# Performance work log

Measured on AMD Instinct MI355X. Metric: run time of the kernel, lower is better.

## Reference

```python
import jax, jax.numpy as jnp
from jax import lax
import numpy as np

B, N, XS, LAT = 16, 400000, 256, 10


def setup_inputs() -> dict:
    key = jax.random.key(0)
    ks = jax.random.split(key, 9)
    flow = 2.0 * jax.random.normal(ks[0], (B, N, 3), jnp.float32)
    x = jax.random.normal(ks[1], (B, XS, XS), jnp.float32)
    values = jax.random.normal(ks[2], (N,), jnp.float32)
    # near-identity rotation matrices so most splatted points stay in-grid
    rotations = jnp.eye(3, dtype=jnp.float32)[None] + 0.05 * jax.random.normal(ks[3], (B, 3, 3), jnp.float32)
    shifts = 2.0 * jax.random.normal(ks[4], (B, 2), jnp.float32)
    w1 = 0.001 * jax.random.normal(ks[5], (XS * XS, LAT), jnp.float32)
    b1 = jnp.zeros((LAT,), jnp.float32)
    w2 = 0.1 * jax.random.normal(ks[6], (LAT, 2), jnp.float32)
    b2 = jnp.zeros((2,), jnp.float32)
    inds = jax.random.randint(ks[7], (N, 3), 0, XS, dtype=jnp.int32)
    return dict(flow=flow, x=x, values=values, rotations=rotations, shifts=shifts,
                w1=w1, b1=b1, w2=w2, b2=b2, inds=inds, xsize=XS)


def _gaussian_blur3(imgs):
    # dm_pix.gaussian_blur(sigma=1.0, kernel_size=3): separable, SAME (zero) padding
    g = jnp.exp(jnp.asarray(-0.5, imgs.dtype))
    k = jnp.stack([g, jnp.asarray(1.0, imgs.dtype), g])
    k = k / k.sum()
    xi = imgs[:, None]  # (B,1,H,W)
    kh = k.reshape(1, 1, 3, 1)
    kw = k.reshape(1, 1, 1, 3)
    xi = lax.conv_general_dilated(xi, kh, (1, 1), 'SAME')
    xi = lax.conv_general_dilated(xi, kw, (1, 1), 'SAME')
    return xi[:, 0]


def reference(flow, x, values, rotations, shifts, w1, b1, w2, b2, inds, xsize):
    factor = 0.5 * xsize
    # (1,N,3) coords in (z->x order as in source), center, deform
    coords = jnp.stack([inds[:, 2], inds[:, 1], inds[:, 0]], axis=1)[None].astype(flow.dtype)
    coords = coords - factor + flow                       # (B,N,3)
    coords = jnp.einsum('bnc,brc->bnr', coords, rotations)  # coords @ R^T
    coords = coords[..., :2] - shifts[:, None, :] + factor  # (B,N,2)
    c_sampling = jnp.stack([coords[..., 1], coords[..., 0]], axis=2)  # swap -> (row, col)

    bamp = values[None, :]                                # (1,N) broadcast over B
    bposf = jnp.floor(c_sampling)
    bposi = bposf.astype(jnp.int32)                       # (B,N,2)
    frac = c_sampling - bposf                             # fractional parts
    f0, f1 = frac[:, :, 0], frac[:, :, 1]
    a0 = bamp * (1.0 - f0) * (1.0 - f1)
    a1 = bamp * f0 * (1.0 - f1)
    a2 = bamp * f0 * f1
    a3 = bamp * (1.0 - f0) * f1
    bamp_all = jnp.concatenate([a0, a1, a2, a3], axis=1)  # (B,4N)
    bposi_all = jnp.concatenate([bposi,
                                 bposi + jnp.array((1, 0), jnp.int32),
                                 bposi + jnp.array((1, 1), jnp.int32),
                                 bposi + jnp.array((0, 1), jnp.int32)], axis=1)  # (B,4N,2)

    images = jnp.zeros((flow.shape[0], xsize, xsize), flow.dtype)

    def scatter_img(image, pos_i, amp_i):
        return image.at[pos_i[:, 0], pos_i[:, 1]].add(amp_i)

    images = jax.vmap(scatter_img)(images, bposi_all, bamp_all)
    images = _gaussian_blur3(images)

    # ImageAdjustment: per-image scalar gain/offset from conditioning image x
    h = jax.nn.relu(x.reshape(x.shape[0], -1) @ w1 + b1)
    ab = h @ w2 + b2                                      # (B,2)
    a, b = ab[:, 0], ab[:, 1]
    images = a[:, None, None] * images + b[:, None, None]
    # ctf_type == 'none' -> ctfFilter skipped
    return images
```

## Files before the change

kernel.cpp:

```cpp
#include <hip/hip_runtime.h>

#define XS     256
#define XS2    65536
#define LAT    10
#define BR     8
#define NG     (XS / BR)
#define NBINS  512
#define P1     4096
#define K_MAX  7
#define BINCAP 15360
#define SPLIT  2
#define CELLW  128
#define QS     256.0f
#define INVQS  (1.0f / 256.0f)

__device__ __forceinline__ void lds_add_u64(unsigned long long* p,
                                            unsigned long long v) {
    __hip_atomic_fetch_add(p, v, __ATOMIC_RELAXED, __HIP_MEMORY_SCOPE_WORKGROUP);
}

__device__ __forceinline__ unsigned long long pack4(int q0, int q1, int q2, int q3) {
    return (unsigned long long)((long long)q0 + ((long long)q1 << 16) +
                                ((long long)q2 << 32) + ((long long)q3 << 48));
}

__device__ __forceinline__ void compute_rc(const float* __restrict__ flow,
                                           const int* __restrict__ inds,
                                           const float* __restrict__ rot,
                                           const float* __restrict__ shifts,
                                           int b, int n, int N,
                                           int& r, int& c, float& f0, float& f1) {
    const float* R = rot + b * 9;
    float r00 = R[0], r01 = R[1], r02 = R[2];
    float r10 = R[3], r11 = R[4], r12 = R[5];
    float s0 = shifts[b * 2 + 0], s1 = shifts[b * 2 + 1];
    size_t fo = ((size_t)b * N + n) * 3;
    float fw0 = flow[fo + 0], fw1 = flow[fo + 1], fw2 = flow[fo + 2];
    float v0 = (float)inds[n * 3 + 2] - 128.0f + fw0;
    float v1 = (float)inds[n * 3 + 1] - 128.0f + fw1;
    float v2 = (float)inds[n * 3 + 0] - 128.0f + fw2;
    float p0 = fmaf(v0, r00, fmaf(v1, r01, fmaf(v2, r02, 128.0f - s0)));
    float p1 = fmaf(v0, r10, fmaf(v1, r11, fmaf(v2, r12, 128.0f - s1)));
    float cs0 = p1, cs1 = p0;
    float ff0 = floorf(cs0), ff1 = floorf(cs1);
    r = (int)ff0; c = (int)ff1;
    f0 = cs0 - ff0; f1 = cs1 - ff1;
}

__device__ __forceinline__ void corner_q(int* __restrict__ Q, int rr, int cc, float a) {
    if (rr >= -XS && rr < XS && cc >= -XS && cc < XS) {
        int q = __float2int_rn(a * QS);
        if (q) atomicAdd(&Q[((rr + XS) & (XS - 1)) * XS + ((cc + XS) & (XS - 1))], q);
    }
}

__device__ __forceinline__ bool is_fast(int r) {
    return (r >= -XS) && (r <= XS - 2) && (r != -1);
}

__device__ __forceinline__ void rec_fallback_q(unsigned long long rec, int bin,
                                               int* __restrict__ qimg) {
    unsigned w = (unsigned)rec;
    float amp = __uint_as_float((unsigned)(rec >> 32));
    int b = bin >> 5, g = bin & 31;
    int rig = w & 7, wc = (w >> 3) & 255;
    int wr = g * BR + rig;
    float f0 = (float)((w >> 13) & 511) * (1.0f / 512.0f);
    float f1 = (float)((w >> 22) & 511) * (1.0f / 512.0f);
    float g0 = 1.0f - f0, g1 = 1.0f - f1;
    int* Q = qimg + (size_t)b * XS2;
    if (w & (1u << 11)) {
        int q00 = __float2int_rn(amp * g0 * g1 * QS);
        int q10 = __float2int_rn(amp * f0 * g1 * QS);
        if (q00) atomicAdd(&Q[wr * XS + wc], q00);
        if (q10) atomicAdd(&Q[(wr + 1) * XS + wc], q10);
    }
    if (w & (1u << 12)) {
        int wc1 = (wc + 1) & 255;
        int q01 = __float2int_rn(amp * g0 * f1 * QS);
        int q11 = __float2int_rn(amp * f0 * f1 * QS);
        if (q01) atomicAdd(&Q[wr * XS + wc1], q01);
        if (q11) atomicAdd(&Q[(wr + 1) * XS + wc1], q11);
    }
}

__global__ void init_kernel(uint4* __restrict__ p, int n4) {
    int i = blockIdx.x * blockDim.x + threadIdx.x;
    int stride = gridDim.x * blockDim.x;
    uint4 z; z.x = 0u; z.y = 0u; z.z = 0u; z.w = 0u;
    for (; i < n4; i += stride) p[i] = z;
}

__device__ __forceinline__ void mlp_block(const float* __restrict__ x,
                                          const float* __restrict__ w1,
                                          float* __restrict__ hraw, int id) {
    int t = threadIdx.x;
    int b = id / LAT, l = id - b * LAT;
    const float* xb = x + (size_t)b * XS2;
    float acc = 0.0f;
#pragma unroll 8
    for (int j = 0; j < 256; j++) {
        int e = j * 256 + t;
        acc += xb[e] * w1[(size_t)e * LAT + l];
    }
#pragma unroll
    for (int off = 32; off > 0; off >>= 1) acc += __shfl_down(acc, off);
    __shared__ float red[4];
    if ((t & 63) == 0) red[t >> 6] = acc;
    __syncthreads();
    if (t == 0) hraw[b * LAT + l] = (red[0] + red[1]) + (red[2] + red[3]);
}

__global__ void __launch_bounds__(256, 6)
place_kernel(const float* __restrict__ flow,
             const float* __restrict__ values,
             const int* __restrict__ inds,
             const float* __restrict__ rot,
             const float* __restrict__ shifts,
             const float* __restrict__ x,
             const float* __restrict__ w1,
             float* __restrict__ hraw,
             unsigned* __restrict__ gcursor,
             unsigned long long* __restrict__ recs,
             int* __restrict__ qimg,
             int N, int TI, int IPB, int B) {
    int t = threadIdx.x;

    if (blockIdx.x >= P1) {
        mlp_block(x, w1, hraw, blockIdx.x - P1);
        return;
    }

    __shared__ unsigned lcnt[NBINS];
    __shared__ unsigned lbase[NBINS];
    lcnt[t] = 0; lcnt[t + 256] = 0;
    __syncthreads();

    unsigned long long rec[K_MAX];
    unsigned meta[K_MAX];
    int s = blockIdx.x * IPB;
    int e = min(s + IPB, TI);
    int b0 = s / N;
    int bBound = (b0 + 1) * N;

#pragma unroll
    for (int k = 0; k < K_MAX; k++) {
        meta[k] = 0xFFFFFFFFu;
        int i = s + t + k * 256;
        if (i < e) {
            int b = (i < bBound) ? b0 : b0 + 1;
            int n = i - b * N;
            int r, c; float f0, f1;
            compute_rc(flow, inds, rot, shifts, b, n, N, r, c, f0, f1);
            float amp = values[n];
            if (is_fast(r)) {
                int wr = (r + XS) & (XS - 1);
                int wc = c & (XS - 1);
                unsigned cv0 = (c >= -XS && c < XS) ? 1u : 0u;
                unsigned cv1 = (c + 1 >= -XS && c + 1 < XS) ? 1u : 0u;
                unsigned q0 = min(511u, (unsigned)(f0 * 512.0f + 0.5f));
                unsigned q1 = min(511u, (unsigned)(f1 * 512.0f + 0.5f));
                unsigned word = (unsigned)(wr & 7) | ((unsigned)wc << 3) |
                                (cv0 << 11) | (cv1 << 12) | (q0 << 13) | (q1 << 22);
                int bin = b * NG + (wr >> 3);
                unsigned rank = atomicAdd(&lcnt[bin], 1u);
                meta[k] = (unsigned)bin | (rank << 9);
                rec[k] = ((unsigned long long)__float_as_uint(amp) << 32) | word;
            } else {
                float g0 = 1.0f - f0, g1 = 1.0f - f1;
                int* Q = qimg + (size_t)b * XS2;
                corner_q(Q, r,     c,     amp * g0 * g1);
                corner_q(Q, r + 1, c,     amp * f0 * g1);
                corner_q(Q, r + 1, c + 1, amp * f0 * f1);
                corner_q(Q, r,     c + 1, amp * g0 * f1);
            }
        }
    }
    __syncthreads();

    for (int bin = t; bin < NBINS; bin += 256) {
        unsigned cn = lcnt[bin];
        lbase[bin] = cn ? atomicAdd(&gcursor[bin], cn) : 0u;
    }
    __syncthreads();

#pragma unroll
    for (int k = 0; k < K_MAX; k++) {
        unsigned m = meta[k];
        if (m != 0xFFFFFFFFu) {
            unsigned bin = m & (NBINS - 1);
            unsigned idx = lbase[bin] + (m >> 9);
            if (idx < BINCAP) recs[(size_t)bin * BINCAP + idx] = rec[k];
            else rec_fallback_q(rec[k], (int)bin, qimg);
        }
    }
}

__global__ void __launch_bounds__(256)
accum_kernel(const unsigned long long* __restrict__ recs,
             const unsigned* __restrict__ gcursor,
             float* __restrict__ reps,
             float* __restrict__ aprons, int B) {
    int bin = blockIdx.x >> 1, sp = blockIdx.x & 1;
    int b = bin >> 5, g = bin & 31;
    __shared__ unsigned long long teven[BR * CELLW];
    __shared__ unsigned long long todd[BR * CELLW];
    int t = threadIdx.x;
    for (int k = t; k < BR * CELLW; k += 256) { teven[k] = 0ull; todd[k] = 0ull; }
    __syncthreads();

    unsigned cnt = min(gcursor[bin], (unsigned)BINCAP);
    unsigned lo = (unsigned)(((unsigned long long)cnt * sp) / SPLIT);
    unsigned hi = (unsigned)(((unsigned long long)cnt * (sp + 1)) / SPLIT);
    const unsigned long long* rb = recs + (size_t)bin * BINCAP;

    for (unsigned i = lo + t; i < hi; i += 256) {
        unsigned long long rc = rb[i];
        unsigned w = (unsigned)rc;
        float amp = __uint_as_float((unsigned)(rc >> 32));
        int rig = w & 7, wc = (w >> 3) & 255;
        float f0 = (float)((w >> 13) & 511) * (1.0f / 512.0f);
        float f1 = (float)((w >> 22) & 511) * (1.0f / 512.0f);
        float g0 = 1.0f - f0, g1 = 1.0f - f1;
        bool cv0 = (w >> 11) & 1, cv1 = (w >> 12) & 1;
        int q00 = cv0 ? __float2int_rn(amp * g0 * g1 * QS) : 0;
        int q10 = cv0 ? __float2int_rn(amp * f0 * g1 * QS) : 0;
        int q01 = cv1 ? __float2int_rn(amp * g0 * f1 * QS) : 0;
        int q11 = cv1 ? __float2int_rn(amp * f0 * f1 * QS) : 0;
        unsigned long long inc = pack4(q00, q10, q01, q11);
        unsigned long long* tile = (wc & 1) ? todd : teven;
        lds_add_u64(&tile[rig * CELLW + (wc >> 1)], inc);
    }
    __syncthreads();

    int c = t;
    int je = c >> 1;
    int jo = (c & 1) ? (c >> 1) : (((c + 254) & 255) >> 1);
    bool e_lo = (c & 1) == 0;
    bool o_lo = (c & 1) == 1;
    float* rep = reps + ((size_t)sp * B + b) * XS2;
    float carry = 0.0f;
#pragma unroll
    for (int rig = 0; rig < BR; rig++) {
        long long se = (long long)teven[rig * CELLW + je];
        int e0 = (int)(short)(se & 0xffff); se = (se - e0) >> 16;
        int e1 = (int)(short)(se & 0xffff); se = (se - e1) >> 16;
        int e2 = (int)(short)(se & 0xffff); se = (se - e2) >> 16;
        int e3 = (int)se;
        long long so = (long long)todd[rig * CELLW + jo];
        int o0 = (int)(short)(so & 0xffff); so = (so - o0) >> 16;
        int o1 = (int)(short)(so & 0xffff); so = (so - o1) >> 16;
        int o2 = (int)(short)(so & 0xffff); so = (so - o2) >> 16;
        int o3 = (int)so;
        float r0 = (e_lo ? (float)e0 : (float)e2) + (o_lo ? (float)o0 : (float)o2);
        float r1 = (e_lo ? (float)e1 : (float)e3) + (o_lo ? (float)o1 : (float)o3);
        rep[(g * BR + rig) * XS + c] = (carry + r0) * INVQS;
        carry = r1;
    }
    aprons[((size_t)bin * 2 + sp) * XS + c] = carry * INVQS;
}

__global__ void scatter_kernel(const float* __restrict__ flow,
                               const float* __restrict__ values,
                               const int* __restrict__ inds,
                               const float* __restrict__ rot,
                               const float* __restrict__ shifts,
                               int* __restrict__ qimg, int N) {
    int b = blockIdx.y;
    int n = blockIdx.x * blockDim.x + threadIdx.x;
    if (n >= N) return;
    int r, c; float f0, f1;
    compute_rc(flow, inds, rot, shifts, b, n, N, r, c, f0, f1);
    float amp = values[n];
    float g0 = 1.0f - f0, g1 = 1.0f - f1;
    int* Q = qimg + (size_t)b * XS2;
    corner_q(Q, r,     c,     amp * g0 * g1);
    corner_q(Q, r + 1, c,     amp * f0 * g1);
    corner_q(Q, r + 1, c + 1, amp * f0 * f1);
    corner_q(Q, r,     c + 1, amp * g0 * f1);
}

__global__ void mlp_kernel(const float* __restrict__ x,
                           const float* __restrict__ w1,
                           float* __restrict__ hraw) {
    mlp_block(x, w1, hraw, blockIdx.x);
}

__device__ __forceinline__ float S_load(const int* __restrict__ qimg,
                                        const float* __restrict__ reps,
                                        const float* __restrict__ aprons,
                                        int B, int b, int row, int c, int fast) {
    size_t o = (size_t)b * XS2 + row * XS + c;
    float v = (float)qimg[o] * INVQS;
    if (fast) {
        v += reps[o] + reps[(size_t)B * XS2 + o];
        if (row > 0 && (row & 7) == 0) {
            size_t bin = (size_t)b * NG + ((row >> 3) - 1);
            v += aprons[bin * 2 * XS + c] + aprons[(bin * 2 + 1) * XS + c];
        }
    }
    return v;
}

__global__ void blur_kernel(const int* __restrict__ qimg,
                            const float* __restrict__ reps,
                            const float* __restrict__ aprons,
                            const float* __restrict__ hraw,
                            const float* __restrict__ b1,
                            const float* __restrict__ w2,
                            const float* __restrict__ b2,
                            float* __restrict__ out, int B, int fast) {
    int b = blockIdx.y, r = blockIdx.x, c = threadIdx.x;
    float av = b2[0], bv = b2[1];
#pragma unroll
    for (int l = 0; l < LAT; l++) {
        float h = hraw[b * LAT + l] + b1[l];
        h = h > 0.0f ? h : 0.0f;
        av += h * w2[l * 2 + 0];
        bv += h * w2[l * 2 + 1];
    }
    const float g   = 0.6065306597126334f;
    const float inv = 1.0f / (1.0f + 2.0f * g);
    float up  = (r > 0)      ? S_load(qimg, reps, aprons, B, b, r - 1, c, fast) : 0.0f;
    float mid =                S_load(qimg, reps, aprons, B, b, r,     c, fast);
    float dn  = (r < XS - 1) ? S_load(qimg, reps, aprons, B, b, r + 1, c, fast) : 0.0f;
    float v = (g * (up + dn) + mid) * inv;
    __shared__ float row[XS + 2];
    row[c + 1] = v;
    if (c == 0) { row[0] = 0.0f; row[XS + 1] = 0.0f; }
    __syncthreads();
    float hh = (g * (row[c] + row[c + 2]) + v) * inv;
    out[(size_t)b * XS2 + (size_t)r * XS + c] = av * hh + bv;
}

extern "C" void kernel_launch(void* const* d_in, const int* in_sizes, int n_in,
                              void* d_out, int out_size, void* d_ws, size_t ws_size,
                              hipStream_t stream) {
    const float* flow   = (const float*)d_in[0];
    const float* x      = (const float*)d_in[1];
    const float* values = (const float*)d_in[2];
    const float* rot    = (const float*)d_in[3];
    const float* shifts = (const float*)d_in[4];
    const float* w1     = (const float*)d_in[5];
    const float* b1     = (const float*)d_in[6];
    const float* w2     = (const float*)d_in[7];
    const float* b2     = (const float*)d_in[8];
    const int*   inds   = (const int*)d_in[9];

    int N = in_sizes[2];
    int B = in_sizes[4] / 2;
    int TI  = B * N;
    int IPB = (TI + P1 - 1) / P1;

    size_t imgElems = (size_t)B * XS2;
    int*      qimg    = (int*)d_ws;
    float*    hraw    = (float*)(qimg + imgElems);
    unsigned* gcursor = (unsigned*)(hraw + 256);
    unsigned long long* recs = (unsigned long long*)(gcursor + NBINS);
    float*    reps    = (float*)(recs + (size_t)NBINS * BINCAP);
    float*    aprons  = reps + 2 * imgElems;
    size_t needed = (size_t)((char*)(aprons + (size_t)NBINS * 2 * XS) - (char*)d_ws);

    bool fast = (B * NG == NBINS) && (ws_size >= needed) && (IPB <= K_MAX * 256);

    int n4 = (int)((imgElems * sizeof(int) + 1024 + NBINS * 4) / 16);
    init_kernel<<<512, 256, 0, stream>>>((uint4*)d_ws, n4);

    if (fast) {
        place_kernel<<<P1 + B * LAT, 256, 0, stream>>>(flow, values, inds, rot, shifts,
                                                       x, w1, hraw, gcursor, recs, qimg,
                                                       N, TI, IPB, B);
        accum_kernel<<<NBINS * SPLIT, 256, 0, stream>>>(recs, gcursor, reps, aprons, B);
    } else {
        dim3 g1((N + 255) / 256, B);
        scatter_kernel<<<g1, 256, 0, stream>>>(flow, values, inds, rot, shifts, qimg, N);
        mlp_kernel<<<B * LAT, 256, 0, stream>>>(x, w1, hraw);
    }

    dim3 g3(XS, B);
    blur_kernel<<<g3, XS, 0, stream>>>(qimg, reps, aprons, hraw, b1, w2, b2,
                                       (float*)d_out, B, fast ? 1 : 0);
}
```

Baseline: 246.1 us.

## Stage binned records in LDS and write them contiguously per bin

The place kernel now keeps its records in LDS and uses a 64-bin local counter covering only the two batch images a block can touch. After a wave-level prefix scan it rebuilds the records grouped by bin, so the global stores become contiguous runs per bin instead of scattered 8-byte writes. The MLP blocks now launch first, and the occupancy hint in launch_bounds is removed. The change costs about 30 KB of LDS per block, which may lower occupancy, and adds an extra LDS pass and barrier. It also assumes IPB stays within RECSL.

```diff
diff --git a/kernel.cpp b/kernel.cpp
--- a/kernel.cpp
+++ b/kernel.cpp
@@ -8,6 +8,8 @@
 #define NBINS  512
 #define P1     4096
 #define K_MAX  7
+#define SLOTS  1792
+#define RECSL  1568
 #define BINCAP 15360
 #define SPLIT  2
 #define CELLW  128
@@ -111,7 +113,7 @@
     if (t == 0) hraw[b * LAT + l] = (red[0] + red[1]) + (red[2] + red[3]);
 }
 
-__global__ void __launch_bounds__(256, 6)
+__global__ void __launch_bounds__(256)
 place_kernel(const float* __restrict__ flow,
              const float* __restrict__ values,
              const int* __restrict__ inds,
@@ -126,27 +128,32 @@
              int N, int TI, int IPB, int B) {
     int t = threadIdx.x;
 
-    if (blockIdx.x >= P1) {
-        mlp_block(x, w1, hraw, blockIdx.x - P1);
+    if (blockIdx.x < (unsigned)(B * LAT)) {
+        mlp_block(x, w1, hraw, blockIdx.x);
         return;
     }
-
-    __shared__ unsigned lcnt[NBINS];
-    __shared__ unsigned lbase[NBINS];
-    lcnt[t] = 0; lcnt[t + 256] = 0;
-    __syncthreads();
-
-    unsigned long long rec[K_MAX];
-    unsigned meta[K_MAX];
-    int s = blockIdx.x * IPB;
+    int bid = blockIdx.x - B * LAT;
+
+    __shared__ unsigned long long recL[SLOTS];
+    __shared__ unsigned long long recS[RECSL];
+    __shared__ unsigned char bins8[SLOTS];
+    __shared__ unsigned char binR8[RECSL];
+    __shared__ unsigned lcnt[64];
+    __shared__ unsigned sbase[64];
+    __shared__ unsigned lbase[64];
+
+    if (t < 64) lcnt[t] = 0;
+    __syncthreads();
+
+    int s = bid * IPB;
     int e = min(s + IPB, TI);
     int b0 = s / N;
     int bBound = (b0 + 1) * N;
 
-#pragma unroll
     for (int k = 0; k < K_MAX; k++) {
-        meta[k] = 0xFFFFFFFFu;
-        int i = s + t + k * 256;
+        int slot = k * 256 + t;
+        int i = s + slot;
+        unsigned char bl = 0xFF;
         if (i < e) {
             int b = (i < bBound) ? b0 : b0 + 1;
             int n = i - b * N;
@@ -162,10 +169,10 @@
                 unsigned q1 = min(511u, (unsigned)(f1 * 512.0f + 0.5f));
                 unsigned word = (unsigned)(wr & 7) | ((unsigned)wc << 3) |
                                 (cv0 << 11) | (cv1 << 12) | (q0 << 13) | (q1 << 22);
-                int bin = b * NG + (wr >> 3);
-                unsigned rank = atomicAdd(&lcnt[bin], 1u);
-                meta[k] = (unsigned)bin | (rank << 9);
-                rec[k] = ((unsigned long long)__float_as_uint(amp) << 32) | word;
+                int local = (b - b0) * NG + (wr >> 3);
+                atomicAdd(&lcnt[local], 1u);
+                recL[slot] = ((unsigned long long)__float_as_uint(amp) << 32) | word;
+                bl = (unsigned char)local;
             } else {
                 float g0 = 1.0f - f0, g1 = 1.0f - f1;
                 int* Q = qimg + (size_t)b * XS2;
@@ -175,24 +182,46 @@
                 corner_q(Q, r,     c + 1, amp * g0 * f1);
             }
         }
-    }
-    __syncthreads();
-
-    for (int bin = t; bin < NBINS; bin += 256) {
-        unsigned cn = lcnt[bin];
-        lbase[bin] = cn ? atomicAdd(&gcursor[bin], cn) : 0u;
-    }
-    __syncthreads();
-
+        bins8[slot] = bl;
+    }
+    __syncthreads();
+
+    if (t < 64) {
+        unsigned cn = lcnt[t];
+        unsigned gb = 0;
+        if (cn) gb = atomicAdd(&gcursor[b0 * NG + t], cn);
+        lbase[t] = gb;
+        unsigned sc = cn;
 #pragma unroll
+        for (int off = 1; off < 64; off <<= 1) {
+            unsigned nv = __shfl_up(sc, off, 64);
+            if (t >= off) sc += nv;
+        }
+        sbase[t] = sc - cn;
+        lcnt[t] = 0;
+    }
+    __syncthreads();
+
     for (int k = 0; k < K_MAX; k++) {
-        unsigned m = meta[k];
-        if (m != 0xFFFFFFFFu) {
-            unsigned bin = m & (NBINS - 1);
-            unsigned idx = lbase[bin] + (m >> 9);
-            if (idx < BINCAP) recs[(size_t)bin * BINCAP + idx] = rec[k];
-            else rec_fallback_q(rec[k], (int)bin, qimg);
+        int slot = k * 256 + t;
+        unsigned bl = bins8[slot];
+        if (bl != 0xFFu) {
+            unsigned r2 = atomicAdd(&lcnt[bl], 1u);
+            unsigned q = sbase[bl] + r2;
+            recS[q] = recL[slot];
+            binR8[q] = (unsigned char)bl;
         }
+    }
+    __syncthreads();
+
+    unsigned total = sbase[63] + lcnt[63];
+    for (unsigned p = t; p < total; p += 256) {
+        unsigned long long rc = recS[p];
+        unsigned bl = binR8[p];
+        unsigned idx = lbase[bl] + (p - sbase[bl]);
+        int bing = b0 * NG + (int)bl;
+        if (idx < BINCAP) recs[(size_t)bing * BINCAP + idx] = rc;
+        else rec_fallback_q(rc, bing, qimg);
     }
 }
 
@@ -361,7 +390,7 @@
     float*    aprons  = reps + 2 * imgElems;
     size_t needed = (size_t)((char*)(aprons + (size_t)NBINS * 2 * XS) - (char*)d_ws);
 
-    bool fast = (B * NG == NBINS) && (ws_size >= needed) && (IPB <= K_MAX * 256);
+    bool fast = (B * NG == NBINS) && (ws_size >= needed) && (IPB <= RECSL);
 
     int n4 = (int)((imgElems * sizeof(int) + 1024 + NBINS * 4) / 16);
     init_kernel<<<512, 256, 0, stream>>>((uint4*)d_ws, n4);
```

Measured after the change: 216.7 us. 1.14x faster.

## Stage per-batch records in LDS and write bins out contiguously

Applied to the files above, without the earlier changes.

Place blocks now each cover one batch image (512 blocks per image) and keep records in shared-memory slots per row-bin instead of registers. After a per-bin global cursor reservation and a shuffle prefix scan, threads copy records out in a compacted order, so consecutive threads write consecutive addresses within a bin. This is meant to turn scattered 8-byte global stores into coalesced ones and drop the K_MAX register arrays so occupancy can rise to 8 waves per SIMD. The cost is extra LDS use, a binary search per output record, and more overflow traffic through the fallback path if a bin exceeds 64 records per block.

```diff
diff --git a/kernel.cpp b/kernel.cpp
--- a/kernel.cpp
+++ b/kernel.cpp
@@ -6,8 +6,8 @@
 #define BR     8
 #define NG     (XS / BR)
 #define NBINS  512
-#define P1     4096
-#define K_MAX  7
+#define SBB    512
+#define CAPB   64
 #define BINCAP 15360
 #define SPLIT  2
 #define CELLW  128
@@ -111,7 +111,7 @@
     if (t == 0) hraw[b * LAT + l] = (red[0] + red[1]) + (red[2] + red[3]);
 }
 
-__global__ void __launch_bounds__(256, 6)
+__global__ void __launch_bounds__(256, 8)
 place_kernel(const float* __restrict__ flow,
              const float* __restrict__ values,
              const int* __restrict__ inds,
@@ -123,76 +123,99 @@
              unsigned* __restrict__ gcursor,
              unsigned long long* __restrict__ recs,
              int* __restrict__ qimg,
-             int N, int TI, int IPB, int B) {
+             int N, int IPB, int B) {
     int t = threadIdx.x;
 
-    if (blockIdx.x >= P1) {
-        mlp_block(x, w1, hraw, blockIdx.x - P1);
+    if (blockIdx.x < (unsigned)(B * LAT)) {
+        mlp_block(x, w1, hraw, blockIdx.x);
         return;
     }
-
-    __shared__ unsigned lcnt[NBINS];
-    __shared__ unsigned lbase[NBINS];
-    lcnt[t] = 0; lcnt[t + 256] = 0;
-    __syncthreads();
-
-    unsigned long long rec[K_MAX];
-    unsigned meta[K_MAX];
-    int s = blockIdx.x * IPB;
-    int e = min(s + IPB, TI);
-    int b0 = s / N;
-    int bBound = (b0 + 1) * N;
-
+    int bid = blockIdx.x - B * LAT;
+    int b = bid >> 9;
+    int j = bid & (SBB - 1);
+
+    __shared__ unsigned long long slots[NG * CAPB];
+    __shared__ unsigned lcnt[NG];
+    __shared__ unsigned sbase[NG];
+    __shared__ unsigned lbase[NG];
+    if (t < NG) lcnt[t] = 0;
+    __syncthreads();
+
+    int s = b * N + j * IPB;
+    int e = min(s + IPB, (b + 1) * N);
+
+    const float* R = rot + b * 9;
+    float r00 = R[0], r01 = R[1], r02 = R[2];
+    float r10 = R[3], r11 = R[4], r12 = R[5];
+    float s0 = shifts[b * 2 + 0], s1 = shifts[b * 2 + 1];
+    int* Q = qimg + (size_t)b * XS2;
+
+    for (int i = s + t; i < e; i += 256) {
+        int n = i - b * N;
+        size_t fo = (size_t)i * 3;
+        float fw0 = flow[fo + 0], fw1 = flow[fo + 1], fw2 = flow[fo + 2];
+        float v0 = (float)inds[n * 3 + 2] - 128.0f + fw0;
+        float v1 = (float)inds[n * 3 + 1] - 128.0f + fw1;
+        float v2 = (float)inds[n * 3 + 0] - 128.0f + fw2;
+        float p0 = fmaf(v0, r00, fmaf(v1, r01, fmaf(v2, r02, 128.0f - s0)));
+        float p1 = fmaf(v0, r10, fmaf(v1, r11, fmaf(v2, r12, 128.0f - s1)));
+        float ff0 = floorf(p1), ff1 = floorf(p0);
+        int r = (int)ff0, c = (int)ff1;
+        float f0 = p1 - ff0, f1 = p0 - ff1;
+        float amp = values[n];
+        if (is_fast(r)) {
+            int wr = (r + XS) & (XS - 1);
+            int wc = c & (XS - 1);
+            unsigned cv0 = (c >= -XS && c < XS) ? 1u : 0u;
+            unsigned cv1 = (c + 1 >= -XS && c + 1 < XS) ? 1u : 0u;
+            unsigned q0 = min(511u, (unsigned)(f0 * 512.0f + 0.5f));
+            unsigned q1 = min(511u, (unsigned)(f1 * 512.0f + 0.5f));
+            unsigned word = (unsigned)(wr & 7) | ((unsigned)wc << 3) |
+                            (cv0 << 11) | (cv1 << 12) | (q0 << 13) | (q1 << 22);
+            unsigned long long rec =
+                ((unsigned long long)__float_as_uint(amp) << 32) | word;
+            int local = wr >> 3;
+            unsigned r2 = atomicAdd(&lcnt[local], 1u);
+            if (r2 < CAPB) slots[local * CAPB + r2] = rec;
+            else rec_fallback_q(rec, b * NG + local, qimg);
+        } else {
+            float g0 = 1.0f - f0, g1 = 1.0f - f1;
+            corner_q(Q, r,     c,     amp * g0 * g1);
+            corner_q(Q, r + 1, c,     amp * f0 * g1);
+            corner_q(Q, r + 1, c + 1, amp * f0 * f1);
+            corner_q(Q, r,     c + 1, amp * g0 * f1);
+        }
+    }
+    __syncthreads();
+
+    if (t < NG) {
+        unsigned cn = min(lcnt[t], (unsigned)CAPB);
+        unsigned gb = cn ? atomicAdd(&gcursor[b * NG + t], cn) : 0u;
+        lbase[t] = gb;
+        lcnt[t] = cn;
+        unsigned sc = cn;
 #pragma unroll
-    for (int k = 0; k < K_MAX; k++) {
-        meta[k] = 0xFFFFFFFFu;
-        int i = s + t + k * 256;
-        if (i < e) {
-            int b = (i < bBound) ? b0 : b0 + 1;
-            int n = i - b * N;
-            int r, c; float f0, f1;
-            compute_rc(flow, inds, rot, shifts, b, n, N, r, c, f0, f1);
-            float amp = values[n];
-            if (is_fast(r)) {
-                int wr = (r + XS) & (XS - 1);
-                int wc = c & (XS - 1);
-                unsigned cv0 = (c >= -XS && c < XS) ? 1u : 0u;
-                unsigned cv1 = (c + 1 >= -XS && c + 1 < XS) ? 1u : 0u;
-                unsigned q0 = min(511u, (unsigned)(f0 * 512.0f + 0.5f));
-                unsigned q1 = min(511u, (unsigned)(f1 * 512.0f + 0.5f));
-                unsigned word = (unsigned)(wr & 7) | ((unsigned)wc << 3) |
-                                (cv0 << 11) | (cv1 << 12) | (q0 << 13) | (q1 << 22);
-                int bin = b * NG + (wr >> 3);
-                unsigned rank = atomicAdd(&lcnt[bin], 1u);
-                meta[k] = (unsigned)bin | (rank << 9);
-                rec[k] = ((unsigned long long)__float_as_uint(amp) << 32) | word;
-            } else {
-                float g0 = 1.0f - f0, g1 = 1.0f - f1;
-                int* Q = qimg + (size_t)b * XS2;
-                corner_q(Q, r,     c,     amp * g0 * g1);
-                corner_q(Q, r + 1, c,     amp * f0 * g1);
-                corner_q(Q, r + 1, c + 1, amp * f0 * f1);
-                corner_q(Q, r,     c + 1, amp * g0 * f1);
-            }
+        for (int off = 1; off < NG; off <<= 1) {
+            unsigned nv = __shfl_up(sc, off, NG);
+            if (t >= off) sc += nv;
         }
-    }
-    __syncthreads();
-
-    for (int bin = t; bin < NBINS; bin += 256) {
-        unsigned cn = lcnt[bin];
-        lbase[bin] = cn ? atomicAdd(&gcursor[bin], cn) : 0u;
-    }
-    __syncthreads();
-
-#pragma unroll
-    for (int k = 0; k < K_MAX; k++) {
-        unsigned m = meta[k];
-        if (m != 0xFFFFFFFFu) {
-            unsigned bin = m & (NBINS - 1);
-            unsigned idx = lbase[bin] + (m >> 9);
-            if (idx < BINCAP) recs[(size_t)bin * BINCAP + idx] = rec[k];
-            else rec_fallback_q(rec[k], (int)bin, qimg);
+        sbase[t] = sc - cn;
+    }
+    __syncthreads();
+
+    unsigned total = sbase[NG - 1] + lcnt[NG - 1];
+    for (unsigned p = t; p < total; p += 256) {
+        int lo = 0, hi = NG - 1;
+        while (lo < hi) {
+            int mid = (lo + hi + 1) >> 1;
+            if (sbase[mid] <= p) lo = mid; else hi = mid - 1;
         }
+        unsigned off = p - sbase[lo];
+        unsigned long long rc = slots[lo * CAPB + off];
+        unsigned idx = lbase[lo] + off;
+        int bing = b * NG + lo;
+        if (idx < BINCAP) recs[(size_t)bing * BINCAP + idx] = rc;
+        else rec_fallback_q(rc, bing, qimg);
     }
 }
 
@@ -349,8 +372,7 @@
 
     int N = in_sizes[2];
     int B = in_sizes[4] / 2;
-    int TI  = B * N;
-    int IPB = (TI + P1 - 1) / P1;
+    int IPB = (N + SBB - 1) / SBB;
 
     size_t imgElems = (size_t)B * XS2;
     int*      qimg    = (int*)d_ws;
@@ -361,15 +383,16 @@
     float*    aprons  = reps + 2 * imgElems;
     size_t needed = (size_t)((char*)(aprons + (size_t)NBINS * 2 * XS) - (char*)d_ws);
 
-    bool fast = (B * NG == NBINS) && (ws_size >= needed) && (IPB <= K_MAX * 256);
+    bool fast = (B * NG == NBINS) && (ws_size >= needed);
 
     int n4 = (int)((imgElems * sizeof(int) + 1024 + NBINS * 4) / 16);
     init_kernel<<<512, 256, 0, stream>>>((uint4*)d_ws, n4);
 
     if (fast) {
-        place_kernel<<<P1 + B * LAT, 256, 0, stream>>>(flow, values, inds, rot, shifts,
-                                                       x, w1, hraw, gcursor, recs, qimg,
-                                                       N, TI, IPB, B);
+        place_kernel<<<B * LAT + B * SBB, 256, 0, stream>>>(flow, values, inds, rot,
+                                                            shifts, x, w1, hraw,
+                                                            gcursor, recs, qimg,
+                                                            N, IPB, B);
         accum_kernel<<<NBINS * SPLIT, 256, 0, stream>>>(recs, gcursor, reps, aprons, B);
     } else {
         dim3 g1((N + 255) / 256, B);
```

Result: faster. 214.0 us (-13.0%).
